# Kernel optimization log

Hardware: AMD Instinct MI355X
Metric: run time of the kernel (lower is better)

Reference implementation:

```python
import jax, jax.numpy as jnp
import numpy as np

CUTOFF = 1.0
MAX_NEIGHBORS = 32
ATOMS_PER_MOL = 512  # uniform molecule size (static, jit-friendly)
NUM_MOLS = 256


def setup_inputs() -> dict:
    key = jax.random.key(0)
    B, n = NUM_MOLS, ATOMS_PER_MOL
    atoms_x = jax.random.normal(key, (B * n, 3), dtype=jnp.float32)
    graph_batch = jnp.repeat(jnp.arange(B, dtype=jnp.int32), n)  # [N]
    return {"atoms_x": atoms_x, "graph_batch": graph_batch}


def reference(atoms_x, graph_batch):
    """Radius graph with per-atom top-K nearest neighbors, per molecule.

    Faithful to the torch module under the (static-shape) assumption that
    molecules are uniform size ATOMS_PER_MOL and graph_batch is contiguous.
    Variable-length edge lists are returned padded: invalid slots have
    bond_i = bond_j = -1, bond_vec = 0, bond_dist = 0, plus a validity mask.
    Valid entries match the torch output (row-major per atom, K nearest).
    """
    N = atoms_x.shape[0]
    n = ATOMS_PER_MOL
    B = N // n
    K = MAX_NEIGHBORS
    pos = atoms_x.reshape(B, n, 3)

    # diff[b, i, j] = pos[b, j] - pos[b, i]  (matches torch unsqueeze(0)-unsqueeze(1))
    diff = pos[:, None, :, :] - pos[:, :, None, :]          # [B, n, n, 3]
    d2 = jnp.sum(diff * diff, axis=-1)                       # [B, n, n]
    c2 = jnp.float32(CUTOFF) ** 2
    nbr_mask = (d2 < c2) & (d2 > 0)                          # dist<cutoff & dist>0

    # K smallest masked squared distances per atom (sqrt is monotone -> same topk)
    d2_masked = jnp.where(nbr_mask, d2, jnp.inf)
    _, idx = jax.lax.top_k(-d2_masked, K)                    # [B, n, K] neighbor cols
    valid = jnp.take_along_axis(nbr_mask, idx, axis=2)       # [B, n, K]

    # gather neighbor positions: pos_j[b, i, k] = pos[b, idx[b, i, k]]
    pos_j = jax.vmap(lambda p, ix: p[ix])(pos, idx)          # [B, n, K, 3]
    vec = pos_j - pos[:, :, None, :]                         # pos[dst] - pos[src]
    vec = jnp.where(valid[..., None], vec, 0.0)
    d2k = jnp.sum(vec * vec, axis=-1)
    dist = jnp.sqrt(jnp.where(valid, d2k, 1.0)) * valid      # safe sqrt, zero padding

    mol_base = jnp.arange(B, dtype=jnp.int32)[:, None, None] * n   # [B,1,1]
    row = mol_base + jnp.arange(n, dtype=jnp.int32)[None, :, None]  # global src idx
    bond_i = jnp.where(valid, jnp.broadcast_to(row, idx.shape), -1)
    bond_j = jnp.where(valid, mol_base + idx.astype(jnp.int32), -1)

    E = B * n * K
    return (bond_i.reshape(E), bond_j.reshape(E),
            vec.reshape(E, 3), dist.reshape(E), valid.reshape(E))
```

## Files before the change

### kernel.cpp

```cpp
#include <hip/hip_runtime.h>
#include <cstdint>


#define K_NBR 32
#define MOL_N 512
#define CAND_N 576
typedef unsigned long long u64;
typedef unsigned u32;

#define DPPK(ctrl, v) __builtin_amdgcn_update_dpp(0, (v), (ctrl), 0xF, 0xF, true)
#define SWZK(off, v) __builtin_amdgcn_ds_swizzle((v), (off))

__device__ __forceinline__ int ce(int k, int o, bool up) {
  const u32 a = (u32)k, b = (u32)o;
  const u32 mn = a < b ? a : b;
  const u32 mx = a < b ? b : a;
  return (int)(up ? mx : mn);
}

struct LaneBits {
  bool b1, b2, b4, b8, b16, b32;
  int bp63;
};

__device__ __forceinline__ int bsort64(int k, const LaneBits& L) {
  k = ce(k, DPPK(0xB1, k), L.b1);
  k = ce(k, DPPK(0x1B, k), L.b2);
  k = ce(k, DPPK(0xB1, k), L.b1);
  k = ce(k, DPPK(0x141, k), L.b4);
  k = ce(k, DPPK(0x4E, k), L.b2);
  k = ce(k, DPPK(0xB1, k), L.b1);
  k = ce(k, DPPK(0x140, k), L.b8);
  k = ce(k, SWZK(0x101F, k), L.b4);
  k = ce(k, DPPK(0x4E, k), L.b2);
  k = ce(k, DPPK(0xB1, k), L.b1);
  k = ce(k, SWZK(0x7C1F, k), L.b16);
  k = ce(k, DPPK(0x128, k), L.b8);
  k = ce(k, SWZK(0x101F, k), L.b4);
  k = ce(k, DPPK(0x4E, k), L.b2);
  k = ce(k, DPPK(0xB1, k), L.b1);
  k = ce(k, __builtin_amdgcn_ds_bpermute(L.bp63, k), L.b32);
  k = ce(k, SWZK(0x401F, k), L.b16);
  k = ce(k, DPPK(0x128, k), L.b8);
  k = ce(k, SWZK(0x101F, k), L.b4);
  k = ce(k, DPPK(0x4E, k), L.b2);
  k = ce(k, DPPK(0xB1, k), L.b1);
  return k;
}

__device__ __forceinline__ int merge_low32(int k, int k2, const LaneBits& L) {
  const int krev = SWZK(0x7C1F, k2);
  const u32 a = (u32)k, b = (u32)krev;
  int m = (int)(a < b ? a : b);
  m = ce(m, SWZK(0x401F, m), L.b16);
  m = ce(m, DPPK(0x128, m), L.b8);
  m = ce(m, SWZK(0x101F, m), L.b4);
  m = ce(m, DPPK(0x4E, m), L.b2);
  m = ce(m, DPPK(0xB1, m), L.b1);
  return m;
}

__global__ __launch_bounds__(256) void topo_kernel(
    const float* __restrict__ atoms_x, float* __restrict__ out, int E_i) {
  __shared__ float sx[MOL_N], sy[MOL_N], sz[MOL_N];
  __shared__ u32 cand[4][CAND_N];

  const int tid = threadIdx.x;
  const int lane = tid & 63;
  const int wave = tid >> 6;
  const int mol = blockIdx.x >> 3;
  const int blk = blockIdx.x & 7;
  const size_t E = (size_t)E_i;

  const float* mp = atoms_x + (size_t)mol * (MOL_N * 3);
  for (int e = tid; e < MOL_N * 3; e += 256) {
    float v = mp[e];
    int a = e / 3;
    int c = e - a * 3;
    if (c == 0) sx[a] = v;
    else if (c == 1) sy[a] = v;
    else sz[a] = v;
  }
  __syncthreads();

  float px[8], py[8], pz[8];
#pragma unroll
  for (int s = 0; s < 8; ++s) {
    const int j = lane + (s << 6);
    px[s] = sx[j]; py[s] = sy[j]; pz[s] = sz[j];
  }

  float* o_bi = out;
  float* o_bj = out + E;
  float* o_vec = out + 2 * E;
  float* o_dist = out + 5 * E;
  float* o_val = out + 6 * E;

  u32* wc = cand[wave];
  LaneBits L;
  L.b1 = (lane & 1);  L.b2 = (lane & 2);   L.b4 = (lane & 4);
  L.b8 = (lane & 8);  L.b16 = (lane & 16); L.b32 = (lane & 32);
  L.bp63 = ((lane ^ 63) << 2);

  for (int it = 0; it < 16; ++it) {
    const int i_loc = blk * 64 + wave * 16 + it;
    const int i_glob = mol * MOL_N + i_loc;
    const float xi = sx[i_loc], yi = sy[i_loc], zi = sz[i_loc];

    int base = 0;
#pragma unroll
    for (int s = 0; s < 8; ++s) {
      const float dx = __fsub_rn(px[s], xi);
      const float dy = __fsub_rn(py[s], yi);
      const float dz = __fsub_rn(pz[s], zi);
      const float d2 = __fadd_rn(
          __fadd_rn(__fmul_rn(dx, dx), __fmul_rn(dy, dy)), __fmul_rn(dz, dz));
      const bool pred = (d2 > 0.0f) && (d2 < 1.0f);
      const u64 bal = __ballot(pred);
      const int prefix = (int)__builtin_amdgcn_mbcnt_hi(
          (u32)(bal >> 32), __builtin_amdgcn_mbcnt_lo((u32)bal, 0u));
      const u32 key =
          (__float_as_uint(d2) & 0xFFFFFE00u) | (u32)(lane + (s << 6));
      const int off = pred ? (base + prefix) : (512 + lane);
      wc[off] = key;
      base += (int)__popcll(bal);
    }
    const int C = base;
    __builtin_amdgcn_wave_barrier();

    int k = (lane < C) ? (int)wc[lane] : (int)0xFFFFFFFFu;
    k = bsort64(k, L);
    for (int b0 = 64; b0 < C; b0 += 64) {
      int k2 = (b0 + lane < C) ? (int)wc[b0 + lane] : (int)0xFFFFFFFFu;
      k2 = bsort64(k2, L);
      k = merge_low32(k, k2, L);
    }
    __builtin_amdgcn_wave_barrier();

    if (lane < K_NBR) {
      const u32 key = (u32)k;
      const bool valid = (key != 0xFFFFFFFFu);
      const int j = (int)(key & 511u);
      const int jj = valid ? j : i_loc;
      const float vx = __fsub_rn(sx[jj], xi);
      const float vy = __fsub_rn(sy[jj], yi);
      const float vz = __fsub_rn(sz[jj], zi);
      const float d2e = __fadd_rn(
          __fadd_rn(__fmul_rn(vx, vx), __fmul_rn(vy, vy)), __fmul_rn(vz, vz));
      const size_t e = (size_t)i_glob * K_NBR + (size_t)lane;
      o_bi[e] = valid ? (float)i_glob : -1.0f;
      o_bj[e] = valid ? (float)(mol * MOL_N + j) : -1.0f;
      o_vec[e * 3 + 0] = valid ? vx : 0.0f;
      o_vec[e * 3 + 1] = valid ? vy : 0.0f;
      o_vec[e * 3 + 2] = valid ? vz : 0.0f;
      o_dist[e] = valid ? sqrtf(d2e) : 0.0f;
      o_val[e] = valid ? 1.0f : 0.0f;
    }
  }
}

extern "C" void kernel_launch(void* const* d_in, const int* in_sizes, int n_in,
                              void* d_out, int out_size, void* d_ws,
                              size_t ws_size, hipStream_t stream) {
  const float* atoms_x = (const float*)d_in[0];
  const int N = in_sizes[0] / 3;
  const int E = out_size / 7;
  const int blocks = N / 64;
  topo_kernel<<<blocks, 256, 0, stream>>>(atoms_x, (float*)d_out, E);
}
```

Baseline: 161.9 us.

## Skip 64-wide sort stages for small candidate sets and reuse key distance

Result: faster. 153.9 us (-4.9%).

```diff
diff --git a/kernel.cpp b/kernel.cpp
--- a/kernel.cpp
+++ b/kernel.cpp
@@ -4,7 +4,6 @@
 
 #define K_NBR 32
 #define MOL_N 512
-#define CAND_N 576
 typedef unsigned long long u64;
 typedef unsigned u32;
 
@@ -23,7 +22,7 @@
   int bp63;
 };
 
-__device__ __forceinline__ int bsort64(int k, const LaneBits& L) {
+__device__ __forceinline__ int bsort32_prefix(int k, const LaneBits& L) {
   k = ce(k, DPPK(0xB1, k), L.b1);
   k = ce(k, DPPK(0x1B, k), L.b2);
   k = ce(k, DPPK(0xB1, k), L.b1);
@@ -39,6 +38,10 @@
   k = ce(k, SWZK(0x101F, k), L.b4);
   k = ce(k, DPPK(0x4E, k), L.b2);
   k = ce(k, DPPK(0xB1, k), L.b1);
+  return k;
+}
+
+__device__ __forceinline__ int bsort64_suffix(int k, const LaneBits& L) {
   k = ce(k, __builtin_amdgcn_ds_bpermute(L.bp63, k), L.b32);
   k = ce(k, SWZK(0x401F, k), L.b16);
   k = ce(k, DPPK(0x128, k), L.b8);
@@ -63,7 +66,7 @@
 __global__ __launch_bounds__(256) void topo_kernel(
     const float* __restrict__ atoms_x, float* __restrict__ out, int E_i) {
   __shared__ float sx[MOL_N], sy[MOL_N], sz[MOL_N];
-  __shared__ u32 cand[4][CAND_N];
+  __shared__ u32 cand[4][MOL_N];
 
   const int tid = threadIdx.x;
   const int lane = tid & 63;
@@ -88,6 +91,10 @@
   for (int s = 0; s < 8; ++s) {
     const int j = lane + (s << 6);
     px[s] = sx[j]; py[s] = sy[j]; pz[s] = sz[j];
+  }
+#pragma unroll
+  for (int s = 0; s < 8; ++s) {
+    asm volatile("" : "+v"(px[s]), "+v"(py[s]), "+v"(pz[s]));
   }
 
   float* o_bi = out;
@@ -115,25 +122,28 @@
       const float dz = __fsub_rn(pz[s], zi);
       const float d2 = __fadd_rn(
           __fadd_rn(__fmul_rn(dx, dx), __fmul_rn(dy, dy)), __fmul_rn(dz, dz));
-      const bool pred = (d2 > 0.0f) && (d2 < 1.0f);
+      const u32 db = __float_as_uint(d2);
+      const bool pred = (db - 1u) < 0x3F7FFFFFu;
       const u64 bal = __ballot(pred);
       const int prefix = (int)__builtin_amdgcn_mbcnt_hi(
           (u32)(bal >> 32), __builtin_amdgcn_mbcnt_lo((u32)bal, 0u));
-      const u32 key =
-          (__float_as_uint(d2) & 0xFFFFFE00u) | (u32)(lane + (s << 6));
-      const int off = pred ? (base + prefix) : (512 + lane);
-      wc[off] = key;
+      if (pred)
+        wc[base + prefix] = (db & 0xFFFFFE00u) | (u32)(lane + (s << 6));
       base += (int)__popcll(bal);
     }
     const int C = base;
     __builtin_amdgcn_wave_barrier();
 
     int k = (lane < C) ? (int)wc[lane] : (int)0xFFFFFFFFu;
-    k = bsort64(k, L);
-    for (int b0 = 64; b0 < C; b0 += 64) {
-      int k2 = (b0 + lane < C) ? (int)wc[b0 + lane] : (int)0xFFFFFFFFu;
-      k2 = bsort64(k2, L);
-      k = merge_low32(k, k2, L);
+    k = bsort32_prefix(k, L);
+    if (C > 32) {
+      k = bsort64_suffix(k, L);
+      for (int b0 = 64; b0 < C; b0 += 64) {
+        int k2 = (b0 + lane < C) ? (int)wc[b0 + lane] : (int)0xFFFFFFFFu;
+        k2 = bsort32_prefix(k2, L);
+        k2 = bsort64_suffix(k2, L);
+        k = merge_low32(k, k2, L);
+      }
     }
     __builtin_amdgcn_wave_barrier();
 
@@ -145,15 +155,15 @@
       const float vx = __fsub_rn(sx[jj], xi);
       const float vy = __fsub_rn(sy[jj], yi);
       const float vz = __fsub_rn(sz[jj], zi);
-      const float d2e = __fadd_rn(
-          __fadd_rn(__fmul_rn(vx, vx), __fmul_rn(vy, vy)), __fmul_rn(vz, vz));
+      const float d2t = __uint_as_float(key & 0xFFFFFE00u);
+      const float dist = __builtin_amdgcn_sqrtf(d2t);
       const size_t e = (size_t)i_glob * K_NBR + (size_t)lane;
       o_bi[e] = valid ? (float)i_glob : -1.0f;
       o_bj[e] = valid ? (float)(mol * MOL_N + j) : -1.0f;
       o_vec[e * 3 + 0] = valid ? vx : 0.0f;
       o_vec[e * 3 + 1] = valid ? vy : 0.0f;
       o_vec[e * 3 + 2] = valid ? vz : 0.0f;
-      o_dist[e] = valid ? sqrtf(d2e) : 0.0f;
+      o_dist[e] = valid ? dist : 0.0f;
       o_val[e] = valid ? 1.0f : 0.0f;
     }
   }
```
